# Kernel tuning notes

Hardware: AMD Instinct MI355X
Metric: run time of the kernel (lower is better)

Reference implementation:

```python
import jax, jax.numpy as jnp
import numpy as np

GAMMA = 2.0
K_NEIGH = 10
N = 8192
F_IN = 512     # recon_fea_dim
F_HID = 512    # graph_h_dim
F_OUT = 256    # graph_out_dim
N_CLU = 10     # cluster_num


def setup_inputs() -> dict:
    key = jax.random.key(0)
    ks = jax.random.split(key, 8)
    x = jax.random.normal(ks[0], (N, F_IN), dtype=jnp.float32)
    # GCN layer 1 (selu activation, skip connection)
    W1 = jax.random.normal(ks[1], (F_IN, F_HID), dtype=jnp.float32) * (1.0 / np.sqrt(F_IN))
    b1 = jnp.zeros((F_HID,), dtype=jnp.float32)
    skip1 = jnp.ones((F_HID,), dtype=jnp.float32)
    # GCN layer 2 (identity activation, skip connection)
    W2 = jax.random.normal(ks[2], (F_HID, F_OUT), dtype=jnp.float32) * (1.0 / np.sqrt(F_HID))
    b2 = jnp.zeros((F_OUT,), dtype=jnp.float32)
    skip2 = jnp.ones((F_OUT,), dtype=jnp.float32)
    # MGC transform: Linear(graph_out_dim -> n_clusters)
    Wt = jax.random.normal(ks[3], (N_CLU, F_OUT), dtype=jnp.float32) * (1.0 / np.sqrt(F_OUT))
    bt = jnp.zeros((N_CLU,), dtype=jnp.float32)
    return {"x": x, "W1": W1, "b1": b1, "skip1": skip1,
            "W2": W2, "b2": b2, "skip2": skip2, "Wt": Wt, "bt": bt}


def _build_knn_graph(x):
    # pairwise squared distance via gram trick (same math as (x_i - x_j)**2 sum)
    sq = jnp.sum(x * x, axis=1)                       # [N]
    d2 = sq[:, None] + sq[None, :] - 2.0 * (x @ x.T)  # [N, N]
    S = jnp.exp(-d2 / GAMMA)
    S = jnp.where(jnp.eye(S.shape[0], dtype=bool), -jnp.inf, S)
    _, idx = jax.lax.top_k(S, K_NEIGH)                # [N, K]
    n = S.shape[0]
    rows = jnp.broadcast_to(jnp.arange(n)[:, None], idx.shape)
    A = jnp.zeros((n, n), dtype=jnp.float32)
    A = A.at[rows, idx].set(1.0)
    A = A.at[idx, rows].set(1.0)                      # symmetrize
    rowsum = jnp.sum(A, axis=1)
    inv = jnp.where(rowsum > 0, 1.0 / rowsum, 0.0)
    A_hat = A * inv[:, None]                          # D^{-1} A
    return A, A_hat


def _gcn_layer(h, A_hat, W, b, skip, act):
    out = h @ W
    out = out * skip + A_hat @ out                    # fused skip + aggregation
    out = out + b
    return act(out)


def reference(x, W1, b1, skip1, W2, b2, skip2, Wt, bt):
    A, A_hat = _build_knn_graph(x)
    # GCN encode: gc1 (selu) -> relu -> gc2 (identity)
    h = _gcn_layer(x, A_hat, W1, b1, skip1, jax.nn.selu)
    h = jax.nn.relu(h)
    emb = _gcn_layer(h, A_hat, W2, b2, skip2, lambda v: v)  # [N, F_OUT]
    # MGC spectral clustering loss
    assign = jax.nn.softmax(emb @ Wt.T + bt, axis=1)  # [N, C]
    deg = jnp.sum(A, axis=0)[:, None]                 # [N, 1]
    n_edges = jnp.sum(deg)
    graph_pooled = (A @ assign).T @ assign            # [C, C]
    norm_l = assign.T @ deg                           # [C, 1]
    norm_r = deg.T @ assign                           # [1, C]
    normalizer = (norm_l @ norm_r) / 2.0 / n_edges
    spectral_loss = -jnp.trace(graph_pooled - normalizer) / 2.0 / n_edges
    return spectral_loss
```

## Files before the change

### kernel.cpp

```cpp
#include <hip/hip_runtime.h>
#include <math.h>
#include <stdint.h>

#define NPTS 8192
#define FIN 512
#define FHID 512
#define FOUT 256
#define NCLU 10
#define KNEI 10
#define LISTCAP 4160

typedef __attribute__((ext_vector_type(4))) float f32x4;
typedef __attribute__((ext_vector_type(8))) short bf16x8;

__device__ __forceinline__ unsigned short bf16_rne(float f) {
    union { float f; unsigned u; } c; c.f = f;
    return (unsigned short)((c.u + 0x7FFFu + ((c.u >> 16) & 1u)) >> 16);
}
__device__ __forceinline__ float bf16_to_f(unsigned short h) {
    union { unsigned u; float f; } c; c.u = ((unsigned)h) << 16;
    return c.f;
}

__global__ void k_sumsq(const float* __restrict__ x, float* __restrict__ sq) {
    int row = blockIdx.x;
    const float* xr = x + (size_t)row * FIN;
    float s = 0.f;
    for (int k = threadIdx.x; k < FIN; k += 256) s += xr[k] * xr[k];
    __shared__ float red[256];
    red[threadIdx.x] = s; __syncthreads();
    for (int off = 128; off > 0; off >>= 1) {
        if (threadIdx.x < off) red[threadIdx.x] += red[threadIdx.x + off];
        __syncthreads();
    }
    if (threadIdx.x == 0) sq[row] = red[0];
}

__global__ void k_split(const float* __restrict__ in, unsigned short* __restrict__ hi,
                        unsigned short* __restrict__ lo) {
    int i = blockIdx.x * 256 + threadIdx.x;
    f32x4 v = reinterpret_cast<const f32x4*>(in)[i];
    ushort4 h, l;
    #pragma unroll
    for (int e = 0; e < 4; e++) {
        unsigned short hb = bf16_rne(v[e]);
        ((unsigned short*)&h)[e] = hb;
        ((unsigned short*)&l)[e] = bf16_rne(v[e] - bf16_to_f(hb));
    }
    reinterpret_cast<ushort4*>(hi)[i] = h;
    reinterpret_cast<ushort4*>(lo)[i] = l;
}

__global__ __launch_bounds__(256) void k_wtrans(const float* __restrict__ W,
        unsigned short* __restrict__ TH, unsigned short* __restrict__ TL, int K, int N) {
    __shared__ float t[32][33];
    int k0 = blockIdx.y * 32, n0 = blockIdx.x * 32;
    int ln = threadIdx.x & 31, lt = threadIdx.x >> 5;
    #pragma unroll
    for (int q = 0; q < 4; q++)
        t[lt + q * 8][ln] = W[(size_t)(k0 + lt + q * 8) * N + n0 + ln];
    __syncthreads();
    #pragma unroll
    for (int q = 0; q < 4; q++) {
        float v = t[ln][lt + q * 8];
        unsigned short hb = bf16_rne(v);
        size_t o = (size_t)(n0 + lt + q * 8) * K + k0 + ln;
        TH[o] = hb;
        TL[o] = bf16_rne(v - bf16_to_f(hb));
    }
}

#define GR_ROWS 128
#define GR_TW 128
#define GR_CHUNKS 8
#define GR_CHUNK_COLS (NPTS / GR_CHUNKS)
#define GR_TILES_PER_CHUNK (GR_CHUNK_COLS / GR_TW)
#define GR_STEPS (GR_TILES_PER_CHUNK * 8)

__global__ __launch_bounds__(512, 2) void k_gram_topk(
    const unsigned short* __restrict__ xb, const float* __restrict__ sq,
    float* __restrict__ tpv, int* __restrict__ tpi)
{
    __shared__ short Bl[2][128][64];
    __shared__ float tval[GR_ROWS][KNEI];
    __shared__ int   tidxs[GR_ROWS][KNEI];

    const int tid  = threadIdx.x;
    const int lane = tid & 63;
    const int wv   = tid >> 6;
    const int rg   = blockIdx.x >> 3;
    const int ch   = blockIdx.x & 7;
    const int r0   = rg * GR_ROWS;
    const int cbase = ch * GR_CHUNK_COLS;

    for (int e = tid; e < GR_ROWS * KNEI; e += 512) {
        tval[e / KNEI][e % KNEI] = -INFINITY;
        tidxs[e / KNEI][e % KNEI] = 0x7fffffff;
    }

    const int arow  = r0 + wv * 16 + (lane & 15);
    const int akoff = (lane >> 4) * 8;
    bf16x8 afr[16];
    #pragma unroll
    for (int ks = 0; ks < 16; ks++)
        afr[ks] = *reinterpret_cast<const bf16x8*>(xb + (size_t)arow * FIN + ks * 32 + akoff);

    float si_r[4];
    #pragma unroll
    for (int r = 0; r < 4; r++) si_r[r] = sq[r0 + wv * 16 + (lane >> 4) * 4 + r];

    const int stg_row = tid >> 2, stg_seg = tid & 3;

    bf16x8 pre[2];
    {
        const unsigned short* src = xb + (size_t)(cbase + stg_row) * FIN + stg_seg * 16;
        #pragma unroll
        for (int q = 0; q < 2; q++) pre[q] = *reinterpret_cast<const bf16x8*>(src + q * 8);
        #pragma unroll
        for (int q = 0; q < 2; q++) {
            int g = stg_seg * 2 + q;
            *reinterpret_cast<bf16x8*>(&Bl[0][stg_row][(g ^ (stg_row & 7)) * 8]) = pre[q];
        }
    }
    __syncthreads();

    f32x4 acc[8];
    for (int u = 0; u < GR_STEPS; ++u) {
        const int t  = u >> 3, kc = u & 7;
        const int c0 = cbase + t * GR_TW;
        const int cur = u & 1;

        if (kc == 0) {
            #pragma unroll
            for (int ct = 0; ct < 8; ct++) acc[ct] = (f32x4){0.f, 0.f, 0.f, 0.f};
        }

        if (u < GR_STEPS - 1) {
            const int u2 = u + 1, t2 = u2 >> 3, kc2 = u2 & 7;
            const unsigned short* src = xb + (size_t)(cbase + t2 * GR_TW + stg_row) * FIN + kc2 * 64 + stg_seg * 16;
            #pragma unroll
            for (int q = 0; q < 2; q++) pre[q] = *reinterpret_cast<const bf16x8*>(src + q * 8);
        }

        #pragma unroll
        for (int ksl = 0; ksl < 2; ++ksl) {
            #pragma unroll
            for (int ct = 0; ct < 8; ct++) {
                const int cl = ct * 16 + (lane & 15);
                const int q = ksl * 4 + (lane >> 4);
                bf16x8 bfr = *reinterpret_cast<const bf16x8*>(&Bl[cur][cl][(q ^ (cl & 7)) * 8]);
                acc[ct] = __builtin_amdgcn_mfma_f32_16x16x32_bf16(afr[kc * 2 + ksl], bfr, acc[ct], 0, 0, 0);
            }
        }

        if (kc == 7) {
            float sjv[8];
            #pragma unroll
            for (int ct = 0; ct < 8; ct++) sjv[ct] = sq[c0 + ct * 16 + (lane & 15)];

            #pragma unroll
            for (int r = 0; r < 4; ++r) {
                const int row_g = wv * 16 + (lane >> 4) * 4 + r;
                const int gi = r0 + row_g;
                float cvv[8];
                #pragma unroll
                for (int ct = 0; ct < 8; ct++) {
                    const int gj = c0 + ct * 16 + (lane & 15);
                    const float d2 = si_r[r] + sjv[ct] - 2.f * acc[ct][r];
                    cvv[ct] = (gj == gi) ? -INFINITY : expf(-d2 * 0.5f);
                }
                float lv = INFINITY; int lj = -1;
                bool done = false;
                #pragma unroll 1
                for (int m = 0; m < KNEI; ++m) {
                    float bv = -INFINITY; int bj = 0x7fffffff;
                    #pragma unroll
                    for (int ct = 0; ct < 8; ct++) {
                        const int j = c0 + ct * 16 + (lane & 15);
                        const float v = cvv[ct];
                        bool elig = (!done) && (v < lv || (v == lv && j > lj));
                        bool better = elig && (v > bv || (v == bv && j < bj));
                        bv = better ? v : bv;
                        bj = better ? j : bj;
                    }
                    #pragma unroll
                    for (int mm = 1; mm <= 8; mm <<= 1) {
                        float ov = __shfl_xor(bv, mm);
                        int   oj = __shfl_xor(bj, mm);
                        bool take = (ov > bv || (ov == bv && oj < bj));
                        bv = take ? ov : bv;
                        bj = take ? oj : bj;
                    }
                    float t9 = tval[row_g][KNEI - 1];
                    int   i9 = tidxs[row_g][KNEI - 1];
                    bool pass = (!done) && (bv > t9 || (bv == t9 && bj < i9));
                    done = done || !pass;
                    if (__all(done)) break;
                    if (pass && (lane & 15) == 0) {
                        int pp = KNEI - 1;
                        tval[row_g][pp] = bv; tidxs[row_g][pp] = bj;
                        while (pp > 0) {
                            float pv = tval[row_g][pp - 1]; int pi = tidxs[row_g][pp - 1];
                            if (bv > pv || (bv == pv && bj < pi)) {
                                tval[row_g][pp] = pv; tidxs[row_g][pp] = pi;
                                tval[row_g][pp - 1] = bv; tidxs[row_g][pp - 1] = bj;
                                --pp;
                            } else break;
                        }
                    }
                    __builtin_amdgcn_wave_barrier();
                    lv = bv; lj = bj;
                }
            }
        }

        if (u < GR_STEPS - 1) {
            #pragma unroll
            for (int q = 0; q < 2; q++) {
                int g = stg_seg * 2 + q;
                *reinterpret_cast<bf16x8*>(&Bl[cur ^ 1][stg_row][(g ^ (stg_row & 7)) * 8]) = pre[q];
            }
        }
        __syncthreads();
    }

    for (int e = tid; e < GR_ROWS * KNEI; e += 512) {
        int r = e / KNEI, m = e % KNEI;
        size_t o = (((size_t)(r0 + r) * GR_CHUNKS) + ch) * KNEI + m;
        tpv[o] = tval[r][m];
        tpi[o] = tidxs[r][m];
    }
}

__global__ __launch_bounds__(256) void k_topk_merge(const float* __restrict__ tpv,
        const int* __restrict__ tpi, int* __restrict__ topidx) {
    int r = blockIdx.x * 256 + threadIdx.x;
    int p[GR_CHUNKS];
    #pragma unroll
    for (int c = 0; c < GR_CHUNKS; c++) p[c] = 0;
    #pragma unroll
    for (int m = 0; m < KNEI; m++) {
        float bv = -INFINITY; int bi = 0x7fffffff; int bc = 0;
        #pragma unroll
        for (int c = 0; c < GR_CHUNKS; c++) {
            if (p[c] < KNEI) {
                size_t o = (((size_t)r * GR_CHUNKS) + c) * KNEI + p[c];
                float v = tpv[o];
                int idx = tpi[o];
                if (v > bv || (v == bv && idx < bi)) { bv = v; bi = idx; bc = c; }
            }
        }
        topidx[(size_t)r * KNEI + m] = bi;
        p[bc]++;
    }
}

__global__ void k_set_edges(const int* __restrict__ topidx, unsigned int* __restrict__ mask) {
    int t = blockIdx.x * 256 + threadIdx.x;
    if (t >= NPTS * KNEI) return;
    int i = t / KNEI;
    int j = topidx[t];
    atomicOr(&mask[(size_t)i * (NPTS / 32) + (j >> 5)], 1u << (j & 31));
    atomicOr(&mask[(size_t)j * (NPTS / 32) + (i >> 5)], 1u << (i & 31));
}

__global__ void k_degree(const unsigned int* __restrict__ mask, float* __restrict__ degf,
                         float* __restrict__ inv) {
    int i = blockIdx.x, lane = threadIdx.x;
    int c = 0;
    for (int w = lane; w < NPTS / 32; w += 64) c += __popc(mask[(size_t)i * (NPTS / 32) + w]);
    for (int off = 32; off > 0; off >>= 1) c += __shfl_xor(c, off);
    if (lane == 0) {
        float d = (float)c;
        degf[i] = d;
        inv[i] = (c > 0) ? 1.0f / d : 0.0f;
    }
}

__global__ __launch_bounds__(256) void k_gemm_mfma(
    const unsigned short* __restrict__ Ahi, const unsigned short* __restrict__ Alo,
    const unsigned short* __restrict__ BThi, const unsigned short* __restrict__ BTlo,
    float* __restrict__ C, int M, int K, int N)
{
    const int tid = threadIdx.x, lane = tid & 63, wv = tid >> 6;
    const int bx = blockIdx.x, by = blockIdx.y;
    const int arow = by * 64 + wv * 16 + (lane & 15);
    const int koff = (lane >> 4) * 8;

    f32x4 acc[8];
    #pragma unroll
    for (int ct = 0; ct < 8; ct++) acc[ct] = (f32x4){0.f, 0.f, 0.f, 0.f};

    for (int kb = 0; kb < K; kb += 128) {
        bf16x8 ah[4], al[4];
        #pragma unroll
        for (int ksl = 0; ksl < 4; ksl++) {
            ah[ksl] = *reinterpret_cast<const bf16x8*>(Ahi + (size_t)arow * K + kb + ksl * 32 + koff);
            al[ksl] = *reinterpret_cast<const bf16x8*>(Alo + (size_t)arow * K + kb + ksl * 32 + koff);
        }
        #pragma unroll
        for (int ksl = 0; ksl < 4; ksl++) {
            #pragma unroll
            for (int ct = 0; ct < 8; ct++) {
                const int n = bx * 128 + ct * 16 + (lane & 15);
                bf16x8 bh = *reinterpret_cast<const bf16x8*>(BThi + (size_t)n * K + kb + ksl * 32 + koff);
                bf16x8 bl = *reinterpret_cast<const bf16x8*>(BTlo + (size_t)n * K + kb + ksl * 32 + koff);
                acc[ct] = __builtin_amdgcn_mfma_f32_16x16x32_bf16(ah[ksl], bh, acc[ct], 0, 0, 0);
                acc[ct] = __builtin_amdgcn_mfma_f32_16x16x32_bf16(ah[ksl], bl, acc[ct], 0, 0, 0);
                acc[ct] = __builtin_amdgcn_mfma_f32_16x16x32_bf16(al[ksl], bh, acc[ct], 0, 0, 0);
            }
        }
    }
    #pragma unroll
    for (int ct = 0; ct < 8; ct++) {
        const int col = bx * 128 + ct * 16 + (lane & 15);
        #pragma unroll
        for (int r = 0; r < 4; r++) {
            const int row = by * 64 + wv * 16 + (lane >> 4) * 4 + r;
            C[(size_t)row * N + col] = acc[ct][r];
        }
    }
}

__global__ __launch_bounds__(256) void k_colsum(const float* __restrict__ P, float* __restrict__ colsum, int Fd) {
    int f = blockIdx.x * 256 + threadIdx.x;
    int r0 = blockIdx.y * (NPTS / 64);
    float s = 0.f;
    for (int r = 0; r < NPTS / 64; r++) s += P[(size_t)(r0 + r) * Fd + f];
    atomicAdd(&colsum[f], s);
}

template <int ACT>
__global__ __launch_bounds__(256) void k_aggregate(const float* __restrict__ P, float* __restrict__ OUT,
        const float* __restrict__ skip, const float* __restrict__ bias,
        const float* __restrict__ inv, const unsigned int* __restrict__ mask,
        const float* __restrict__ colsum, int Fd) {
    __shared__ unsigned short list[LISTCAP];
    __shared__ int cnt_total;
    __shared__ int pos;
    int i = blockIdx.x, tid = threadIdx.x;
    if (tid == 0) { cnt_total = 0; pos = 0; }
    __syncthreads();
    unsigned int w = mask[(size_t)i * (NPTS / 32) + tid];
    atomicAdd(&cnt_total, __popc(w));
    __syncthreads();
    const int deg = cnt_total;
    const bool comp = deg > 4096;
    unsigned int wm = comp ? ~w : w;
    if (comp && tid == (i >> 5)) wm &= ~(1u << (i & 31));
    while (wm) {
        int b = __ffs(wm) - 1;
        wm &= wm - 1;
        int pp = atomicAdd(&pos, 1);
        list[pp] = (unsigned short)(tid * 32 + b);
    }
    __syncthreads();
    const int n = comp ? (NPTS - 1 - deg) : deg;
    const float vinv = inv[i];
    for (int f = tid; f < Fd; f += 256) {
        float s = 0.f;
        for (int q = 0; q < n; q++) s += P[(size_t)list[q] * Fd + f];
        const float pif = P[(size_t)i * Fd + f];
        const float nb = comp ? (colsum[f] - pif - s) : s;
        float o = pif * skip[f] + vinv * nb + bias[f];
        if (ACT == 1) o = (o > 0.f) ? 1.0507009873554805f * o : 0.f;
        OUT[(size_t)i * Fd + f] = o;
    }
}

__global__ void k_assign(const float* __restrict__ emb, const float* __restrict__ Wt,
                         const float* __restrict__ bt, float* __restrict__ assign) {
    int i = blockIdx.x, lane = threadIdx.x;
    float e[4];
    #pragma unroll
    for (int m = 0; m < 4; m++) e[m] = emb[(size_t)i * FOUT + lane + 64 * m];
    float logit[NCLU];
    #pragma unroll
    for (int c = 0; c < NCLU; c++) {
        float p = 0.f;
        #pragma unroll
        for (int m = 0; m < 4; m++) p = fmaf(e[m], Wt[c * FOUT + lane + 64 * m], p);
        #pragma unroll
        for (int off = 32; off > 0; off >>= 1) p += __shfl_xor(p, off);
        logit[c] = p + bt[c];
    }
    float mx = logit[0];
    #pragma unroll
    for (int c = 1; c < NCLU; c++) mx = fmaxf(mx, logit[c]);
    float sum = 0.f, pr[NCLU];
    #pragma unroll
    for (int c = 0; c < NCLU; c++) { pr[c] = expf(logit[c] - mx); sum += pr[c]; }
    float isum = 1.f / sum;
    if (lane < NCLU) {
        float v = 0.f;
        #pragma unroll
        for (int c = 0; c < NCLU; c++) if (lane == c) v = pr[c];
        assign[(size_t)i * NCLU + lane] = v * isum;
    }
}

__global__ __launch_bounds__(256) void k_stats(const float* __restrict__ assign,
        const float* __restrict__ degf, float* __restrict__ colA,
        float* __restrict__ vvec, float* __restrict__ Esum) {
    __shared__ float sc[NCLU], sv[NCLU], se;
    int tid = threadIdx.x;
    if (tid < NCLU) { sc[tid] = 0.f; sv[tid] = 0.f; }
    if (tid == 0) se = 0.f;
    __syncthreads();
    int i = blockIdx.x * 256 + tid;
    const float d = degf[i];
    const float* ar = assign + (size_t)i * NCLU;
    float ed = d;
    #pragma unroll
    for (int off = 32; off > 0; off >>= 1) ed += __shfl_xor(ed, off);
    if ((tid & 63) == 0) atomicAdd(&se, ed);
    #pragma unroll
    for (int c = 0; c < NCLU; c++) {
        float a = ar[c];
        float av = a * d;
        #pragma unroll
        for (int off = 32; off > 0; off >>= 1) { a += __shfl_xor(a, off); av += __shfl_xor(av, off); }
        if ((tid & 63) == 0) { atomicAdd(&sc[c], a); atomicAdd(&sv[c], av); }
    }
    __syncthreads();
    if (tid < NCLU) { atomicAdd(&colA[tid], sc[tid]); atomicAdd(&vvec[tid], sv[tid]); }
    if (tid == NCLU) atomicAdd(Esum, se);
}

__global__ __launch_bounds__(256) void k_spectral(const unsigned int* __restrict__ mask,
        const float* __restrict__ assign, const float* __restrict__ colA,
        float* __restrict__ Tpart) {
    __shared__ unsigned short list[LISTCAP];
    __shared__ int cnt_total;
    __shared__ int pos;
    __shared__ float red[4][NCLU];
    int i = blockIdx.x, tid = threadIdx.x;
    if (tid == 0) { cnt_total = 0; pos = 0; }
    __syncthreads();
    unsigned int w = mask[(size_t)i * (NPTS / 32) + tid];
    atomicAdd(&cnt_total, __popc(w));
    __syncthreads();
    const int deg = cnt_total;
    const bool comp = deg > 4096;
    unsigned int wm = comp ? ~w : w;
    if (comp && tid == (i >> 5)) wm &= ~(1u << (i & 31));
    while (wm) {
        int b = __ffs(wm) - 1;
        wm &= wm - 1;
        int pp = atomicAdd(&pos, 1);
        list[pp] = (unsigned short)(tid * 32 + b);
    }
    __syncthreads();
    const int n = comp ? (NPTS - 1 - deg) : deg;
    float yc[NCLU];
    #pragma unroll
    for (int c = 0; c < NCLU; c++) yc[c] = 0.f;
    for (int q = tid; q < n; q += 256) {
        const float* aj = assign + (size_t)list[q] * NCLU;
        #pragma unroll
        for (int c = 0; c < NCLU; c++) yc[c] += aj[c];
    }
    #pragma unroll
    for (int c = 0; c < NCLU; c++) {
        #pragma unroll
        for (int off = 32; off > 0; off >>= 1) yc[c] += __shfl_xor(yc[c], off);
    }
    int wv = tid >> 6, lane = tid & 63;
    if (lane == 0) {
        #pragma unroll
        for (int c = 0; c < NCLU; c++) red[wv][c] = yc[c];
    }
    __syncthreads();
    if (tid == 0) {
        const float* ai = assign + (size_t)i * NCLU;
        float t = 0.f;
        #pragma unroll
        for (int c = 0; c < NCLU; c++) {
            float y = red[0][c] + red[1][c] + red[2][c] + red[3][c];
            if (comp) y = colA[c] - ai[c] - y;
            t = fmaf(y, ai[c], t);
        }
        Tpart[i] = t;
    }
}

__global__ __launch_bounds__(256) void k_final(const float* __restrict__ Tpart,
        const float* __restrict__ v, const float* __restrict__ Esum, float* __restrict__ out) {
    __shared__ float red[256];
    int tid = threadIdx.x;
    float s = 0.f;
    for (int i = tid; i < NPTS; i += 256) s += Tpart[i];
    red[tid] = s; __syncthreads();
    for (int off = 128; off > 0; off >>= 1) {
        if (tid < off) red[tid] += red[tid + off];
        __syncthreads();
    }
    if (tid == 0) {
        float E = *Esum;
        float v2 = 0.f;
        for (int c = 0; c < NCLU; c++) v2 += v[c] * v[c];
        float tr_norm = v2 / (2.f * E);
        out[0] = -(red[0] - tr_norm) / (2.f * E);
    }
}

extern "C" void kernel_launch(void* const* d_in, const int* in_sizes, int n_in,
                              void* d_out, int out_size, void* d_ws, size_t ws_size,
                              hipStream_t stream) {
    const float* x     = (const float*)d_in[0];
    const float* W1    = (const float*)d_in[1];
    const float* b1    = (const float*)d_in[2];
    const float* skip1 = (const float*)d_in[3];
    const float* W2    = (const float*)d_in[4];
    const float* b2    = (const float*)d_in[5];
    const float* skip2 = (const float*)d_in[6];
    const float* Wt    = (const float*)d_in[7];
    const float* bt    = (const float*)d_in[8];

    char* ws = (char*)d_ws;
    float* bufA = (float*)ws;
    float* bufB = (float*)(ws + ((size_t)16 << 20));
    unsigned int* mask = (unsigned int*)(ws + ((size_t)32 << 20));
    unsigned short* xlo = (unsigned short*)(ws + ((size_t)40 << 20));
    char* p = ws + ((size_t)48 << 20);
    float* sq     = (float*)p; p += NPTS * 4;
    float* degf   = (float*)p; p += NPTS * 4;
    float* inv    = (float*)p; p += NPTS * 4;
    int*   topidx = (int*)p;   p += (size_t)NPTS * KNEI * 4;
    float* assign = (float*)p; p += (size_t)NPTS * NCLU * 4;
    float* Tpart  = (float*)p; p += NPTS * 4;
    float* Esum    = (float*)p; p += 4;
    float* vvec    = (float*)p; p += NCLU * 4;
    float* colA    = (float*)p; p += NCLU * 4;
    float* colsum1 = (float*)p; p += FHID * 4;
    float* colsum2 = (float*)p; p += FOUT * 4;
    unsigned short* WT1hi = (unsigned short*)p; p += (size_t)FHID * FIN * 2;
    unsigned short* WT1lo = (unsigned short*)p; p += (size_t)FHID * FIN * 2;
    unsigned short* WT2hi = (unsigned short*)p; p += (size_t)FOUT * FHID * 2;
    unsigned short* WT2lo = (unsigned short*)p; p += (size_t)FOUT * FHID * 2;

    unsigned short* xb = (unsigned short*)bufA;
    float* tpv = (float*)bufB;
    int*   tpi = (int*)((char*)bufB + ((size_t)4 << 20));
    unsigned short* hhi = (unsigned short*)bufB;
    float* P2 = bufB + ((size_t)2 << 20);

    hipMemsetAsync(mask, 0, (size_t)NPTS * (NPTS / 32) * 4, stream);
    hipMemsetAsync(Esum, 0, (1 + 2 * NCLU + FHID + FOUT) * sizeof(float), stream);

    k_sumsq<<<NPTS, 256, 0, stream>>>(x, sq);
    k_split<<<(NPTS * FIN / 4) / 256, 256, 0, stream>>>(x, xb, xlo);
    k_wtrans<<<dim3(FHID / 32, FIN / 32), 256, 0, stream>>>(W1, WT1hi, WT1lo, FIN, FHID);
    k_wtrans<<<dim3(FOUT / 32, FHID / 32), 256, 0, stream>>>(W2, WT2hi, WT2lo, FHID, FOUT);

    k_gram_topk<<<(NPTS / GR_ROWS) * GR_CHUNKS, 512, 0, stream>>>(xb, sq, tpv, tpi);
    k_topk_merge<<<NPTS / 256, 256, 0, stream>>>(tpv, tpi, topidx);
    k_set_edges<<<(NPTS * KNEI + 255) / 256, 256, 0, stream>>>(topidx, mask);
    k_degree<<<NPTS, 64, 0, stream>>>(mask, degf, inv);

    k_gemm_mfma<<<dim3(FHID / 128, NPTS / 64), 256, 0, stream>>>(xb, xlo, WT1hi, WT1lo, bufB, NPTS, FIN, FHID);
    k_colsum<<<dim3(FHID / 256, 64), 256, 0, stream>>>(bufB, colsum1, FHID);
    k_aggregate<1><<<NPTS, 256, 0, stream>>>(bufB, bufA, skip1, b1, inv, mask, colsum1, FHID);

    k_split<<<(NPTS * FHID / 4) / 256, 256, 0, stream>>>(bufA, hhi, xlo);
    k_gemm_mfma<<<dim3(FOUT / 128, NPTS / 64), 256, 0, stream>>>(hhi, xlo, WT2hi, WT2lo, P2, NPTS, FHID, FOUT);
    k_colsum<<<dim3(FOUT / 256, 64), 256, 0, stream>>>(P2, colsum2, FOUT);
    k_aggregate<0><<<NPTS, 256, 0, stream>>>(P2, bufA, skip2, b2, inv, mask, colsum2, FOUT);

    k_assign<<<NPTS, 64, 0, stream>>>(bufA, Wt, bt, assign);
    k_stats<<<NPTS / 256, 256, 0, stream>>>(assign, degf, colA, vvec, Esum);
    k_spectral<<<NPTS, 256, 0, stream>>>(mask, assign, colA, Tpart);
    k_final<<<1, 256, 0, stream>>>(Tpart, vvec, Esum, (float*)d_out);
}
```

Baseline: 642.9 us.

## Switch gram/top-k to FP8 MFMA and fuse prep, merge and colsum kernels

The kNN gram matrix is now computed with FP8 (e4m3) MFMA on a new per-row e4m3 copy of x, and each block covers 256 rows with 1024 threads. Squared norms, the bf16 hi/lo split and the fp8 conversion are fused into one row-prep kernel. The top-k merge now sets edge bits directly instead of writing an index array. Column sums are folded into the GEMM epilogue. Together these target gram-matrix compute, launch count and extra memory passes, at the cost of much lower precision in the distances that decide neighbor selection, which may pick different neighbors.

```diff
diff --git a/kernel.cpp b/kernel.cpp
--- a/kernel.cpp
+++ b/kernel.cpp
@@ -12,6 +12,7 @@
 
 typedef __attribute__((ext_vector_type(4))) float f32x4;
 typedef __attribute__((ext_vector_type(8))) short bf16x8;
+typedef long i64g;
 
 __device__ __forceinline__ unsigned short bf16_rne(float f) {
     union { float f; unsigned u; } c; c.f = f;
@@ -21,19 +22,42 @@
     union { unsigned u; float f; } c; c.u = ((unsigned)h) << 16;
     return c.f;
 }
-
-__global__ void k_sumsq(const float* __restrict__ x, float* __restrict__ sq) {
-    int row = blockIdx.x;
-    const float* xr = x + (size_t)row * FIN;
-    float s = 0.f;
-    for (int k = threadIdx.x; k < FIN; k += 256) s += xr[k] * xr[k];
-    __shared__ float red[256];
-    red[threadIdx.x] = s; __syncthreads();
-    for (int off = 128; off > 0; off >>= 1) {
-        if (threadIdx.x < off) red[threadIdx.x] += red[threadIdx.x + off];
-        __syncthreads();
-    }
-    if (threadIdx.x == 0) sq[row] = red[0];
+__device__ __forceinline__ unsigned char f32_to_e4m3(float f) {
+    union { float f; unsigned u; } c; c.f = f;
+    unsigned char s = (unsigned char)((c.u >> 24) & 0x80u);
+    float af = fabsf(f);
+    if (af >= 448.f) return s | 0x7E;
+    if (af < 0.015625f) {
+        int m = (int)(af * 512.f + 0.5f);
+        return s | (unsigned char)m;
+    }
+    int e; float m = frexpf(af, &e);
+    int fi = (int)((m * 2.f - 1.f) * 8.f + 0.5f);
+    int E = e - 1 + 7;
+    if (fi == 8) { fi = 0; E += 1; }
+    if (E > 15) { E = 15; fi = 6; }
+    return s | (unsigned char)((E << 3) | fi);
+}
+
+__global__ __launch_bounds__(256) void k_rowprep(const float* __restrict__ x,
+        float* __restrict__ sq, unsigned short* __restrict__ hi,
+        unsigned short* __restrict__ lo, unsigned char* __restrict__ x8) {
+    __shared__ float red[4];
+    int row = blockIdx.x, tid = threadIdx.x;
+    const float2 v = *reinterpret_cast<const float2*>(x + (size_t)row * FIN + 2 * tid);
+    unsigned short h0 = bf16_rne(v.x), h1 = bf16_rne(v.y);
+    unsigned short l0 = bf16_rne(v.x - bf16_to_f(h0)), l1 = bf16_rne(v.y - bf16_to_f(h1));
+    size_t base = (size_t)row * FIN + 2 * tid;
+    *reinterpret_cast<unsigned*>(hi + base) = (unsigned)h0 | ((unsigned)h1 << 16);
+    *reinterpret_cast<unsigned*>(lo + base) = (unsigned)l0 | ((unsigned)l1 << 16);
+    *reinterpret_cast<unsigned short*>(x8 + base) =
+        (unsigned short)f32_to_e4m3(v.x) | ((unsigned short)f32_to_e4m3(v.y) << 8);
+    float s = v.x * v.x + v.y * v.y;
+    #pragma unroll
+    for (int off = 32; off > 0; off >>= 1) s += __shfl_xor(s, off);
+    if ((tid & 63) == 0) red[tid >> 6] = s;
+    __syncthreads();
+    if (tid == 0) sq[row] = red[0] + red[1] + red[2] + red[3];
 }
 
 __global__ void k_split(const float* __restrict__ in, unsigned short* __restrict__ hi,
@@ -70,18 +94,19 @@
     }
 }
 
-#define GR_ROWS 128
+#define GR_ROWS 256
 #define GR_TW 128
 #define GR_CHUNKS 8
+#define GR_RGRPS (NPTS / GR_ROWS)
 #define GR_CHUNK_COLS (NPTS / GR_CHUNKS)
 #define GR_TILES_PER_CHUNK (GR_CHUNK_COLS / GR_TW)
 #define GR_STEPS (GR_TILES_PER_CHUNK * 8)
 
-__global__ __launch_bounds__(512, 2) void k_gram_topk(
-    const unsigned short* __restrict__ xb, const float* __restrict__ sq,
+__global__ __launch_bounds__(1024) void k_gram_topk(
+    const unsigned char* __restrict__ x8, const float* __restrict__ sq,
     float* __restrict__ tpv, int* __restrict__ tpi)
 {
-    __shared__ short Bl[2][128][64];
+    __shared__ unsigned char Bl[2][128][64];
     __shared__ float tval[GR_ROWS][KNEI];
     __shared__ int   tidxs[GR_ROWS][KNEI];
 
@@ -93,35 +118,27 @@
     const int r0   = rg * GR_ROWS;
     const int cbase = ch * GR_CHUNK_COLS;
 
-    for (int e = tid; e < GR_ROWS * KNEI; e += 512) {
+    for (int e = tid; e < GR_ROWS * KNEI; e += 1024) {
         tval[e / KNEI][e % KNEI] = -INFINITY;
         tidxs[e / KNEI][e % KNEI] = 0x7fffffff;
     }
 
     const int arow  = r0 + wv * 16 + (lane & 15);
     const int akoff = (lane >> 4) * 8;
-    bf16x8 afr[16];
+    i64g afr[16];
     #pragma unroll
     for (int ks = 0; ks < 16; ks++)
-        afr[ks] = *reinterpret_cast<const bf16x8*>(xb + (size_t)arow * FIN + ks * 32 + akoff);
+        afr[ks] = *reinterpret_cast<const i64g*>(x8 + (size_t)arow * FIN + ks * 32 + akoff);
 
     float si_r[4];
     #pragma unroll
     for (int r = 0; r < 4; r++) si_r[r] = sq[r0 + wv * 16 + (lane >> 4) * 4 + r];
 
-    const int stg_row = tid >> 2, stg_seg = tid & 3;
-
-    bf16x8 pre[2];
-    {
-        const unsigned short* src = xb + (size_t)(cbase + stg_row) * FIN + stg_seg * 16;
-        #pragma unroll
-        for (int q = 0; q < 2; q++) pre[q] = *reinterpret_cast<const bf16x8*>(src + q * 8);
-        #pragma unroll
-        for (int q = 0; q < 2; q++) {
-            int g = stg_seg * 2 + q;
-            *reinterpret_cast<bf16x8*>(&Bl[0][stg_row][(g ^ (stg_row & 7)) * 8]) = pre[q];
-        }
-    }
+    const int stg_row = tid >> 3, stg_g = tid & 7;
+
+    i64g pre;
+    pre = *reinterpret_cast<const i64g*>(x8 + (size_t)(cbase + stg_row) * FIN + stg_g * 8);
+    *reinterpret_cast<i64g*>(&Bl[0][stg_row][(stg_g ^ (stg_row & 7)) * 8]) = pre;
     __syncthreads();
 
     f32x4 acc[8];
@@ -137,9 +154,8 @@
 
         if (u < GR_STEPS - 1) {
             const int u2 = u + 1, t2 = u2 >> 3, kc2 = u2 & 7;
-            const unsigned short* src = xb + (size_t)(cbase + t2 * GR_TW + stg_row) * FIN + kc2 * 64 + stg_seg * 16;
-            #pragma unroll
-            for (int q = 0; q < 2; q++) pre[q] = *reinterpret_cast<const bf16x8*>(src + q * 8);
+            pre = *reinterpret_cast<const i64g*>(
+                x8 + (size_t)(cbase + t2 * GR_TW + stg_row) * FIN + kc2 * 64 + stg_g * 8);
         }
 
         #pragma unroll
@@ -148,8 +164,8 @@
             for (int ct = 0; ct < 8; ct++) {
                 const int cl = ct * 16 + (lane & 15);
                 const int q = ksl * 4 + (lane >> 4);
-                bf16x8 bfr = *reinterpret_cast<const bf16x8*>(&Bl[cur][cl][(q ^ (cl & 7)) * 8]);
-                acc[ct] = __builtin_amdgcn_mfma_f32_16x16x32_bf16(afr[kc * 2 + ksl], bfr, acc[ct], 0, 0, 0);
+                i64g bfr = *reinterpret_cast<const i64g*>(&Bl[cur][cl][(q ^ (cl & 7)) * 8]);
+                acc[ct] = __builtin_amdgcn_mfma_f32_16x16x32_fp8_fp8(afr[kc * 2 + ksl], bfr, acc[ct], 0, 0, 0);
             }
         }
 
@@ -215,16 +231,12 @@
         }
 
         if (u < GR_STEPS - 1) {
-            #pragma unroll
-            for (int q = 0; q < 2; q++) {
-                int g = stg_seg * 2 + q;
-                *reinterpret_cast<bf16x8*>(&Bl[cur ^ 1][stg_row][(g ^ (stg_row & 7)) * 8]) = pre[q];
-            }
+            *reinterpret_cast<i64g*>(&Bl[cur ^ 1][stg_row][(stg_g ^ (stg_row & 7)) * 8]) = pre;
         }
         __syncthreads();
     }
 
-    for (int e = tid; e < GR_ROWS * KNEI; e += 512) {
+    for (int e = tid; e < GR_ROWS * KNEI; e += 1024) {
         int r = e / KNEI, m = e % KNEI;
         size_t o = (((size_t)(r0 + r) * GR_CHUNKS) + ch) * KNEI + m;
         tpv[o] = tval[r][m];
@@ -232,8 +244,8 @@
     }
 }
 
-__global__ __launch_bounds__(256) void k_topk_merge(const float* __restrict__ tpv,
-        const int* __restrict__ tpi, int* __restrict__ topidx) {
+__global__ __launch_bounds__(256) void k_merge_edges(const float* __restrict__ tpv,
+        const int* __restrict__ tpi, unsigned int* __restrict__ mask) {
     int r = blockIdx.x * 256 + threadIdx.x;
     int p[GR_CHUNKS];
     #pragma unroll
@@ -250,18 +262,10 @@
                 if (v > bv || (v == bv && idx < bi)) { bv = v; bi = idx; bc = c; }
             }
         }
-        topidx[(size_t)r * KNEI + m] = bi;
         p[bc]++;
-    }
-}
-
-__global__ void k_set_edges(const int* __restrict__ topidx, unsigned int* __restrict__ mask) {
-    int t = blockIdx.x * 256 + threadIdx.x;
-    if (t >= NPTS * KNEI) return;
-    int i = t / KNEI;
-    int j = topidx[t];
-    atomicOr(&mask[(size_t)i * (NPTS / 32) + (j >> 5)], 1u << (j & 31));
-    atomicOr(&mask[(size_t)j * (NPTS / 32) + (i >> 5)], 1u << (i & 31));
+        atomicOr(&mask[(size_t)r * (NPTS / 32) + (bi >> 5)], 1u << (bi & 31));
+        atomicOr(&mask[(size_t)bi * (NPTS / 32) + (r >> 5)], 1u << (r & 31));
+    }
 }
 
 __global__ void k_degree(const unsigned int* __restrict__ mask, float* __restrict__ degf,
@@ -280,12 +284,15 @@
 __global__ __launch_bounds__(256) void k_gemm_mfma(
     const unsigned short* __restrict__ Ahi, const unsigned short* __restrict__ Alo,
     const unsigned short* __restrict__ BThi, const unsigned short* __restrict__ BTlo,
-    float* __restrict__ C, int M, int K, int N)
+    float* __restrict__ C, float* __restrict__ colsum, int M, int K, int N)
 {
+    __shared__ float colpart[128];
     const int tid = threadIdx.x, lane = tid & 63, wv = tid >> 6;
     const int bx = blockIdx.x, by = blockIdx.y;
     const int arow = by * 64 + wv * 16 + (lane & 15);
     const int koff = (lane >> 4) * 8;
+
+    for (int t2 = tid; t2 < 128; t2 += 256) colpart[t2] = 0.f;
 
     f32x4 acc[8];
     #pragma unroll
@@ -311,6 +318,7 @@
             }
         }
     }
+    __syncthreads();
     #pragma unroll
     for (int ct = 0; ct < 8; ct++) {
         const int col = bx * 128 + ct * 16 + (lane & 15);
@@ -319,15 +327,13 @@
             const int row = by * 64 + wv * 16 + (lane >> 4) * 4 + r;
             C[(size_t)row * N + col] = acc[ct][r];
         }
-    }
-}
-
-__global__ __launch_bounds__(256) void k_colsum(const float* __restrict__ P, float* __restrict__ colsum, int Fd) {
-    int f = blockIdx.x * 256 + threadIdx.x;
-    int r0 = blockIdx.y * (NPTS / 64);
-    float s = 0.f;
-    for (int r = 0; r < NPTS / 64; r++) s += P[(size_t)(r0 + r) * Fd + f];
-    atomicAdd(&colsum[f], s);
+        float psum = acc[ct][0] + acc[ct][1] + acc[ct][2] + acc[ct][3];
+        psum += __shfl_xor(psum, 16);
+        psum += __shfl_xor(psum, 32);
+        if ((lane >> 4) == 0) atomicAdd(&colpart[ct * 16 + (lane & 15)], psum);
+    }
+    __syncthreads();
+    if (tid < 128) atomicAdd(&colsum[bx * 128 + tid], colpart[tid]);
 }
 
 template <int ACT>
@@ -526,7 +532,6 @@
     float* sq     = (float*)p; p += NPTS * 4;
     float* degf   = (float*)p; p += NPTS * 4;
     float* inv    = (float*)p; p += NPTS * 4;
-    int*   topidx = (int*)p;   p += (size_t)NPTS * KNEI * 4;
     float* assign = (float*)p; p += (size_t)NPTS * NCLU * 4;
     float* Tpart  = (float*)p; p += NPTS * 4;
     float* Esum    = (float*)p; p += 4;
@@ -542,29 +547,26 @@
     unsigned short* xb = (unsigned short*)bufA;
     float* tpv = (float*)bufB;
     int*   tpi = (int*)((char*)bufB + ((size_t)4 << 20));
+    unsigned char* x8 = (unsigned char*)bufB + ((size_t)8 << 20);
     unsigned short* hhi = (unsigned short*)bufB;
     float* P2 = bufB + ((size_t)2 << 20);
 
     hipMemsetAsync(mask, 0, (size_t)NPTS * (NPTS / 32) * 4, stream);
     hipMemsetAsync(Esum, 0, (1 + 2 * NCLU + FHID + FOUT) * sizeof(float), stream);
 
-    k_sumsq<<<NPTS, 256, 0, stream>>>(x, sq);
-    k_split<<<(NPTS * FIN / 4) / 256, 256, 0, stream>>>(x, xb, xlo);
+    k_rowprep<<<NPTS, 256, 0, stream>>>(x, sq, xb, xlo, x8);
     k_wtrans<<<dim3(FHID / 32, FIN / 32), 256, 0, stream>>>(W1, WT1hi, WT1lo, FIN, FHID);
     k_wtrans<<<dim3(FOUT / 32, FHID / 32), 256, 0, stream>>>(W2, WT2hi, WT2lo, FHID, FOUT);
 
-    k_gram_topk<<<(NPTS / GR_ROWS) * GR_CHUNKS, 512, 0, stream>>>(xb, sq, tpv, tpi);
-    k_topk_merge<<<NPTS / 256, 256, 0, stream>>>(tpv, tpi, topidx);
-    k_set_edges<<<(NPTS * KNEI + 255) / 256, 256, 0, stream>>>(topidx, mask);
+    k_gram_topk<<<GR_RGRPS * GR_CHUNKS, 1024, 0, stream>>>(x8, sq, tpv, tpi);
+    k_merge_edges<<<NPTS / 256, 256, 0, stream>>>(tpv, tpi, mask);
     k_degree<<<NPTS, 64, 0, stream>>>(mask, degf, inv);
 
-    k_gemm_mfma<<<dim3(FHID / 128, NPTS / 64), 256, 0, stream>>>(xb, xlo, WT1hi, WT1lo, bufB, NPTS, FIN, FHID);
-    k_colsum<<<dim3(FHID / 256, 64), 256, 0, stream>>>(bufB, colsum1, FHID);
+    k_gemm_mfma<<<dim3(FHID / 128, NPTS / 64), 256, 0, stream>>>(xb, xlo, WT1hi, WT1lo, bufB, colsum1, NPTS, FIN, FHID);
     k_aggregate<1><<<NPTS, 256, 0, stream>>>(bufB, bufA, skip1, b1, inv, mask, colsum1, FHID);
 
     k_split<<<(NPTS * FHID / 4) / 256, 256, 0, stream>>>(bufA, hhi, xlo);
-    k_gemm_mfma<<<dim3(FOUT / 128, NPTS / 64), 256, 0, stream>>>(hhi, xlo, WT2hi, WT2lo, P2, NPTS, FHID, FOUT);
-    k_colsum<<<dim3(FOUT / 256, 64), 256, 0, stream>>>(P2, colsum2, FOUT);
+    k_gemm_mfma<<<dim3(FOUT / 128, NPTS / 64), 256, 0, stream>>>(hhi, xlo, WT2hi, WT2lo, P2, colsum2, NPTS, FHID, FOUT);
     k_aggregate<0><<<NPTS, 256, 0, stream>>>(P2, bufA, skip2, b2, inv, mask, colsum2, FOUT);
 
     k_assign<<<NPTS, 64, 0, stream>>>(bufA, Wt, bt, assign);
```

Measured after the change: 630.0 us. -2.0%, faster.
